# Performance work log

Hardware: AMD Instinct MI355X
Metric: run time of the kernel (lower is better)

The kernel has to match this reference:

```python
import jax, jax.numpy as jnp
from jax import lax
import numpy as np

RADIUS = 0.3
NSAMPLES = 32
SPATIAL_STRIDE = 32
TKS = 3
TSTRIDE = 2
DIM = 512
DEPTH = 4
HEADS = 8
DIM_HEAD = 64
MLP_DIM = 1024
NUM_CLASSES = 30
B, T, N = 4, 24, 4096


def setup_inputs():
    key = jax.random.key(0)
    ks = jax.random.split(key, 16)
    def w(k, shape, fan_in):
        return jax.random.normal(k, shape, jnp.float32) / np.float32(np.sqrt(fan_in))
    return {
        "xyzs": jax.random.uniform(ks[0], (B, T, N, 3), jnp.float32),
        "old_features": jax.random.normal(ks[1], (B, T, 2, N), jnp.float32),
        "conv_d_w": w(ks[2], (DIM, 4), 4),
        "conv_f_w": w(ks[3], (DIM, 2), 2),
        "pos_w": w(ks[4], (DIM, 4), 4),
        "pos_b": jnp.zeros((DIM,), jnp.float32),
        "contr_w": w(ks[5], (DIM, 4), 4),
        "contr_b": jnp.zeros((DIM,), jnp.float32),
        "ln1_s": jnp.ones((DEPTH, DIM), jnp.float32),
        "ln1_b": jnp.zeros((DEPTH, DIM), jnp.float32),
        "qkv_w": w(ks[6], (DEPTH, 3 * HEADS * DIM_HEAD, DIM), DIM),
        "out_w": w(ks[7], (DEPTH, DIM, HEADS * DIM_HEAD), HEADS * DIM_HEAD),
        "out_b": jnp.zeros((DEPTH, DIM), jnp.float32),
        "ln2_s": jnp.ones((DEPTH, DIM), jnp.float32),
        "ln2_b": jnp.zeros((DEPTH, DIM), jnp.float32),
        "ff1_w": w(ks[8], (DEPTH, MLP_DIM, DIM), DIM),
        "ff1_b": jnp.zeros((DEPTH, MLP_DIM), jnp.float32),
        "ff2_w": w(ks[9], (DEPTH, DIM, MLP_DIM), MLP_DIM),
        "ff2_b": jnp.zeros((DEPTH, DIM), jnp.float32),
        "head_ln_s": jnp.ones((DIM,), jnp.float32),
        "head_ln_b": jnp.zeros((DIM,), jnp.float32),
        "head1_w": w(ks[10], (MLP_DIM, DIM), DIM),
        "head1_b": jnp.zeros((MLP_DIM,), jnp.float32),
        "head2_w": w(ks[11], (NUM_CLASSES, MLP_DIM), MLP_DIM),
        "head2_b": jnp.zeros((NUM_CLASSES,), jnp.float32),
    }


def _fps(xyz, npoint):
    # furthest point sampling, pointnet2 semantics (start at index 0)
    n = xyz.shape[0]
    def body(carry, _):
        dist, last = carry
        d = jnp.sum((xyz - xyz[last]) ** 2, axis=-1)
        dist = jnp.minimum(dist, d)
        nxt = jnp.argmax(dist).astype(jnp.int32)
        return (dist, nxt), nxt
    init = (jnp.full((n,), 1e10, xyz.dtype), jnp.int32(0))
    _, idxs = lax.scan(body, init, None, length=npoint - 1)
    return jnp.concatenate([jnp.zeros((1,), jnp.int32), idxs])


def _ball_query(anchor, neighbor):
    # anchor [M,3], neighbor [N,3] -> [M,NSAMPLES] int32; first-k-in-radius, pad with first hit
    n = neighbor.shape[0]
    d2 = jnp.sum((anchor[:, None, :] - neighbor[None, :, :]) ** 2, axis=-1)
    pos = jnp.where(d2 < RADIUS * RADIUS, jnp.arange(n, dtype=jnp.int32), n)
    idx = -lax.top_k(-pos, NSAMPLES)[0]          # k smallest scan positions
    idx = jnp.where(idx == n, idx[:, :1], idx)   # pad with first found index
    return jnp.where(idx == n, 0, idx)           # nothing in radius -> 0


def _group(pts, idx):
    # pts [B,To,N,C], idx [B,To,M,K] -> [B,To,M,K,C]
    b, to, m, k = idx.shape
    g = jnp.take_along_axis(pts, idx.reshape(b, to, m * k)[..., None], axis=2)
    return g.reshape(b, to, m, k, pts.shape[-1])


def _p4dconv(xyzs, feats, conv_d_w, conv_f_w):
    b, t, n, _ = xyzs.shape
    m = n // SPATIAL_STRIDE
    rad = TKS // 2
    # temporal replicate padding [1,0]
    xyzs_p = jnp.concatenate([xyzs[:, :1], xyzs], axis=1)                             # [B,T+1,N,3]
    feats_p = jnp.concatenate([feats[:, :1], feats], axis=1).transpose(0, 1, 3, 2)    # [B,T+1,N,2]
    t_idx = np.arange(rad, t + 1 - rad, TSTRIDE)                                      # anchor frames (static)
    anchors = xyzs_p[:, t_idx]                                                        # [B,To,N,3]
    fps_idx = jax.vmap(jax.vmap(lambda x: _fps(x, m)))(anchors)                       # [B,To,M]
    anchor_xyz = jnp.take_along_axis(anchors, fps_idx[..., None], axis=2)             # [B,To,M,3]
    pooled = None
    for o in range(-rad, rad + 1):  # temporal kernel (small, structural)
        nb_xyz = xyzs_p[:, t_idx + o]
        nb_feat = feats_p[:, t_idx + o]
        idx = jax.vmap(jax.vmap(_ball_query))(anchor_xyz, nb_xyz)                     # [B,To,M,K]
        disp = _group(nb_xyz, idx) - anchor_xyz[:, :, :, None, :]                     # [B,To,M,K,3]
        disp4 = jnp.concatenate([disp, jnp.full(disp.shape[:-1] + (1,), float(o), disp.dtype)], axis=-1)
        d_emb = jnp.einsum('btmkc,dc->btmkd', disp4, conv_d_w)
        f_emb = jnp.einsum('btmkc,dc->btmkd', _group(nb_feat, idx), conv_f_w)
        feat = jnp.max(f_emb * d_emb, axis=3)                                          # spatial max-pool [B,To,M,D]
        pooled = feat if pooled is None else jnp.maximum(pooled, feat)                 # temporal max-pool
    return anchor_xyz, pooled


def _ln(x, s, b):
    mu = jnp.mean(x, axis=-1, keepdims=True)
    var = jnp.mean((x - mu) ** 2, axis=-1, keepdims=True)
    return (x - mu) / jnp.sqrt(var + 1e-5) * s + b


def reference(xyzs, old_features, conv_d_w, conv_f_w, pos_w, pos_b, contr_w, contr_b,
              ln1_s, ln1_b, qkv_w, out_w, out_b, ln2_s, ln2_b, ff1_w, ff1_b, ff2_w, ff2_b,
              head_ln_s, head_ln_b, head1_w, head1_b, head2_w, head2_b):
    new_xyz, feat = _p4dconv(xyzs, old_features, conv_d_w, conv_f_w)   # [B,To,M,3], [B,To,M,D]
    b, to, m, _ = new_xyz.shape
    tvals = jnp.arange(1, to + 1, dtype=new_xyz.dtype)
    xyzt = jnp.concatenate([new_xyz, jnp.broadcast_to(tvals[None, :, None, None], (b, to, m, 1))], axis=-1)
    xyzts = xyzt.reshape(b, to * m, 4)
    features = feat.reshape(b, to * m, DIM)
    pos = xyzts @ pos_w.T + pos_b                    # Conv1d(4,dim,k=1) == pointwise linear
    contrastive = xyzts @ contr_w.T + contr_b        # Linear(4,dim) on raw [x,y,z,t] tokens
    x = jax.nn.relu(pos + features)
    scale = DIM_HEAD ** -0.5
    for l in range(DEPTH):
        h = _ln(x, ln1_s[l], ln1_b[l])
        qkv = h @ qkv_w[l].T
        q, k, v = jnp.split(qkv, 3, axis=-1)
        q = q.reshape(b, -1, HEADS, DIM_HEAD)
        k = k.reshape(b, -1, HEADS, DIM_HEAD)
        v = v.reshape(b, -1, HEADS, DIM_HEAD)
        att = jax.nn.softmax(jnp.einsum('bihd,bjhd->bhij', q, k) * scale, axis=-1)
        o = jnp.einsum('bhij,bjhd->bihd', att, v).reshape(b, -1, HEADS * DIM_HEAD)
        x = x + o @ out_w[l].T + out_b[l]
        h = _ln(x, ln2_s[l], ln2_b[l])
        x = x + jax.nn.gelu(h @ ff1_w[l].T + ff1_b[l], approximate=False) @ ff2_w[l].T + ff2_b[l]
    pooled = jnp.max(x, axis=1)
    h = _ln(pooled, head_ln_s, head_ln_b)
    logits = jax.nn.gelu(h @ head1_w.T + head1_b, approximate=False) @ head2_w.T + head2_b
    return logits, contrastive, features
```

## Files before the change

### kernel.cpp

```cpp
#include <hip/hip_runtime.h>
#include <math.h>

#define BN_  4
#define TT   24
#define NN   4096
#define TO   12
#define MM   128
#define LL   (TO*MM)
#define BL   (BN_*LL)
#define DM   512
#define NH   8
#define DH   64
#define MLPD 1024
#define NC   30

#define OUT_LOGITS 0
#define OUT_CONTR  (BN_*NC)
#define OUT_FEATS  (OUT_CONTR + BL*DM)

typedef __attribute__((ext_vector_type(8))) short s16x8;
typedef __attribute__((ext_vector_type(4))) float f32x4;
#define MFMA(a,b,c) __builtin_amdgcn_mfma_f32_16x16x32_bf16(a,b,c,0,0,0)

__device__ __forceinline__ void split_bf16(float a, short &h, short &l) {
  unsigned u = __float_as_uint(a);
  h = (short)(u >> 16);
  float ah = __uint_as_float(u & 0xffff0000u);
  float al = a - ah;
  l = (short)(__float_as_uint(al) >> 16);
}

__device__ __forceinline__ void split8(float4 a, float4 b, s16x8 &h8, s16x8 &l8) {
  short h, l;
  split_bf16(a.x,h,l); h8[0]=h; l8[0]=l;
  split_bf16(a.y,h,l); h8[1]=h; l8[1]=l;
  split_bf16(a.z,h,l); h8[2]=h; l8[2]=l;
  split_bf16(a.w,h,l); h8[3]=h; l8[3]=l;
  split_bf16(b.x,h,l); h8[4]=h; l8[4]=l;
  split_bf16(b.y,h,l); h8[5]=h; l8[5]=l;
  split_bf16(b.z,h,l); h8[6]=h; l8[6]=l;
  split_bf16(b.w,h,l); h8[7]=h; l8[7]=l;
}

__device__ __forceinline__ float d2_3(float ax, float ay, float az,
                                      float bx, float by, float bz) {
#pragma clang fp contract(off)
  float dx = ax - bx, dy = ay - by, dz = az - bz;
  float dx2 = dx * dx, dy2 = dy * dy, dz2 = dz * dz;
  return (dx2 + dy2) + dz2;
}

__device__ __forceinline__ float gelu_f(float v) {
  return 0.5f * v * (1.0f + erff(v * 0.70710678118654752440f));
}

__global__ __launch_bounds__(256) void fps_kernel(const float* __restrict__ xyzs,
                                                  float* __restrict__ anchor) {
  __shared__ float sx[NN], sy[NN], sz[NN];
  __shared__ float swv[4];
  __shared__ int   swi[4];
  __shared__ int   s_next;
  int blk = blockIdx.x;
  int b = blk / TO, ti = blk - b * TO;
  int frame = 2 * ti;
  const float* src = xyzs + ((size_t)(b * TT + frame)) * NN * 3;
  int tid = threadIdx.x;
  float dist[16], px[16], py[16], pz[16];
#pragma unroll
  for (int s = 0; s < 16; ++s) {
    int p = tid + s * 256;
    px[s] = src[p * 3 + 0]; py[s] = src[p * 3 + 1]; pz[s] = src[p * 3 + 2];
    sx[p] = px[s]; sy[p] = py[s]; sz[p] = pz[s];
    dist[s] = 1e10f;
  }
  __syncthreads();
  float lx = sx[0], ly = sy[0], lz = sz[0];
  float* aout = anchor + (size_t)blk * MM * 3;
  if (tid == 0) { aout[0] = lx; aout[1] = ly; aout[2] = lz; }
  for (int j = 1; j < MM; ++j) {
    float bestv = -1.0f; int besti = 0;
#pragma unroll
    for (int s = 0; s < 16; ++s) {
      float d2 = d2_3(px[s], py[s], pz[s], lx, ly, lz);
      float dn = fminf(dist[s], d2);
      dist[s] = dn;
      if (dn > bestv) { bestv = dn; besti = tid + s * 256; }
    }
    for (int m = 1; m < 64; m <<= 1) {
      float ov = __shfl_xor(bestv, m, 64);
      int   oi = __shfl_xor(besti, m, 64);
      if (ov > bestv || (ov == bestv && oi < besti)) { bestv = ov; besti = oi; }
    }
    if ((tid & 63) == 0) { swv[tid >> 6] = bestv; swi[tid >> 6] = besti; }
    __syncthreads();
    if (tid == 0) {
      float bv = swv[0]; int bi = swi[0];
      for (int q = 1; q < 4; ++q)
        if (swv[q] > bv || (swv[q] == bv && swi[q] < bi)) { bv = swv[q]; bi = swi[q]; }
      s_next = bi;
      aout[j * 3 + 0] = sx[bi]; aout[j * 3 + 1] = sy[bi]; aout[j * 3 + 2] = sz[bi];
    }
    __syncthreads();
    int nxt = s_next;
    lx = sx[nxt]; ly = sy[nxt]; lz = sz[nxt];
  }
}

__global__ __launch_bounds__(64) void ballconv_kernel(
    const float* __restrict__ xyzs, const float* __restrict__ oldf,
    const float* __restrict__ anchor,
    const float* __restrict__ wdw, const float* __restrict__ wfw,
    float* __restrict__ dout) {
  __shared__ int   sidx[32];
  __shared__ float sdisp[32][4];
  __shared__ float sfeat[32][2];
  int blk = blockIdx.x;
  int b = blk / (TO * MM);
  int rem = blk - b * (TO * MM);
  int ti = rem / MM;
  int lane = threadIdx.x;
  const float* ap = anchor + (size_t)blk * 3;
  float ax = ap[0], ay = ap[1], az = ap[2];
  int d0 = lane * 8;
  float4 wd[8]; float2 wf[8];
#pragma unroll
  for (int jd = 0; jd < 8; ++jd) {
    wd[jd] = *(const float4*)(wdw + (d0 + jd) * 4);
    wf[jd] = *(const float2*)(wfw + (d0 + jd) * 2);
  }
  float fmx[8];
#pragma unroll
  for (int jd = 0; jd < 8; ++jd) fmx[jd] = -INFINITY;

  for (int o = -1; o <= 1; ++o) {
    int tp = 1 + 2 * ti + o;
    int orig = (tp == 0) ? 0 : tp - 1;
    const float* nx = xyzs + ((size_t)(b * TT + orig)) * NN * 3;
    const float* nf = oldf + ((size_t)(b * TT + orig)) * 2 * NN;
    int cnt = 0;
    for (int base = 0; base < NN && cnt < 32; base += 64) {
      int p = base + lane;
      float d2 = d2_3(ax, ay, az, nx[p * 3], nx[p * 3 + 1], nx[p * 3 + 2]);
      bool in = d2 < 0.09f;
      unsigned long long mask = __ballot(in);
      int pos = __popcll(mask & ((1ull << lane) - 1ull));
      if (in && (cnt + pos) < 32) sidx[cnt + pos] = p;
      cnt += __popcll(mask);
    }
    __syncthreads();
    int used = cnt < 32 ? cnt : 32;
    if (lane < 32 && lane >= used) sidx[lane] = (used > 0) ? sidx[0] : 0;
    __syncthreads();
    if (lane < 32) {
      int p = sidx[lane];
      sdisp[lane][0] = nx[p * 3 + 0] - ax;
      sdisp[lane][1] = nx[p * 3 + 1] - ay;
      sdisp[lane][2] = nx[p * 3 + 2] - az;
      sdisp[lane][3] = (float)o;
      sfeat[lane][0] = nf[p];
      sfeat[lane][1] = nf[NN + p];
    }
    __syncthreads();
    for (int k = 0; k < 32; ++k) {
      float p0 = sdisp[k][0], p1 = sdisp[k][1], p2 = sdisp[k][2], p3 = sdisp[k][3];
      float f0 = sfeat[k][0], f1 = sfeat[k][1];
#pragma unroll
      for (int jd = 0; jd < 8; ++jd) {
        float de = wd[jd].x * p0 + wd[jd].y * p1 + wd[jd].z * p2 + wd[jd].w * p3;
        float fe = wf[jd].x * f0 + wf[jd].y * f1;
        fmx[jd] = fmaxf(fmx[jd], fe * de);
      }
    }
    __syncthreads();
  }
  float* fout = dout + OUT_FEATS + (size_t)blk * DM + d0;
#pragma unroll
  for (int jd = 0; jd < 8; jd += 4)
    *(float4*)(fout + jd) = make_float4(fmx[jd], fmx[jd + 1], fmx[jd + 2], fmx[jd + 3]);
}

__global__ __launch_bounds__(256) void posx_kernel(
    const float* __restrict__ anchor,
    const float* __restrict__ pw, const float* __restrict__ pb,
    const float* __restrict__ cw, const float* __restrict__ cb,
    float* __restrict__ dout, float* __restrict__ x) {
  int idx = blockIdx.x * 256 + threadIdx.x;
  int bl = idx >> 9, d = idx & 511;
  int ti = (bl % LL) / MM;
  const float* ap = anchor + (size_t)bl * 3;
  float c0 = ap[0], c1 = ap[1], c2 = ap[2], c3 = (float)(ti + 1);
  float4 pwv = *(const float4*)(pw + d * 4);
  float4 cwv = *(const float4*)(cw + d * 4);
  float pos = pwv.x * c0 + pwv.y * c1 + pwv.z * c2 + pwv.w * c3 + pb[d];
  float con = cwv.x * c0 + cwv.y * c1 + cwv.z * c2 + cwv.w * c3 + cb[d];
  dout[OUT_CONTR + (size_t)idx] = con;
  float v = pos + dout[OUT_FEATS + (size_t)idx];
  x[idx] = v > 0.0f ? v : 0.0f;
}

__global__ __launch_bounds__(64) void ln_split_kernel(
    const float* __restrict__ x, const float* __restrict__ gs,
    const float* __restrict__ gb, short* __restrict__ oh, short* __restrict__ ol) {
  int row = blockIdx.x, lane = threadIdx.x;
  const float* xr = x + (size_t)row * DM + lane * 8;
  float4 v0 = *(const float4*)xr;
  float4 v1 = *(const float4*)(xr + 4);
  float v[8] = {v0.x, v0.y, v0.z, v0.w, v1.x, v1.y, v1.z, v1.w};
  float s = 0.f;
#pragma unroll
  for (int j = 0; j < 8; ++j) s += v[j];
  for (int m = 1; m < 64; m <<= 1) s += __shfl_xor(s, m, 64);
  float mu = s * (1.0f / DM);
  float d[8], ss = 0.f;
#pragma unroll
  for (int j = 0; j < 8; ++j) { d[j] = v[j] - mu; ss += d[j] * d[j]; }
  for (int m = 1; m < 64; m <<= 1) ss += __shfl_xor(ss, m, 64);
  float rs = 1.0f / sqrtf(ss * (1.0f / DM) + 1e-5f);
  const float* gsr = gs + lane * 8;
  const float* gbr = gb + lane * 8;
  s16x8 hv, lv;
#pragma unroll
  for (int j = 0; j < 8; ++j) {
    float f = d[j] * rs * gsr[j] + gbr[j];
    short h, l; split_bf16(f, h, l);
    hv[j] = h; lv[j] = l;
  }
  *(s16x8*)(oh + (size_t)row * DM + lane * 8) = hv;
  *(s16x8*)(ol + (size_t)row * DM + lane * 8) = lv;
}

__global__ __launch_bounds__(64) void ln_kernel(
    const float* __restrict__ x, const float* __restrict__ gs,
    const float* __restrict__ gb, float* __restrict__ out) {
  int row = blockIdx.x, lane = threadIdx.x;
  const float* xr = x + (size_t)row * DM + lane * 8;
  float4 v0 = *(const float4*)xr;
  float4 v1 = *(const float4*)(xr + 4);
  float v[8] = {v0.x, v0.y, v0.z, v0.w, v1.x, v1.y, v1.z, v1.w};
  float s = 0.f;
#pragma unroll
  for (int j = 0; j < 8; ++j) s += v[j];
  for (int m = 1; m < 64; m <<= 1) s += __shfl_xor(s, m, 64);
  float mu = s * (1.0f / DM);
  float d[8], ss = 0.f;
#pragma unroll
  for (int j = 0; j < 8; ++j) { d[j] = v[j] - mu; ss += d[j] * d[j]; }
  for (int m = 1; m < 64; m <<= 1) ss += __shfl_xor(ss, m, 64);
  float rs = 1.0f / sqrtf(ss * (1.0f / DM) + 1e-5f);
  const float* gsr = gs + lane * 8;
  const float* gbr = gb + lane * 8;
  float* orow = out + (size_t)row * DM + lane * 8;
  float r[8];
#pragma unroll
  for (int j = 0; j < 8; ++j) r[j] = d[j] * rs * gsr[j] + gbr[j];
  *(float4*)orow       = make_float4(r[0], r[1], r[2], r[3]);
  *(float4*)(orow + 4) = make_float4(r[4], r[5], r[6], r[7]);
}

template <int EPI>
__global__ __launch_bounds__(256) void mgemm_kernel(
    const short* __restrict__ Ah, const short* __restrict__ Al,
    const float* __restrict__ W,
    const float* __restrict__ bias, const float* __restrict__ res,
    float* __restrict__ Cf, short* __restrict__ Ch, short* __restrict__ Cl,
    int M, int N, int K) {
  __shared__ short As[2][128 * 40];
  __shared__ short Ws[2][128 * 40];
  int tid = threadIdx.x;
  int lane = tid & 63, w = tid >> 6;
  int wr = w >> 1, wc = w & 1;
  int row0 = blockIdx.y * 128, col0 = blockIdx.x * 128;
  int srow = tid >> 1, skc = (tid & 1) * 16;
  const short* Ahp = Ah + (size_t)(row0 + srow) * K + skc;
  const short* Alp = Al + (size_t)(row0 + srow) * K + skc;
  const float* Wp  = W  + (size_t)(col0 + srow) * K + skc;
  int fr = lane & 15, fk = (lane >> 4) * 8;
  f32x4 acc[16];
#pragma unroll
  for (int i = 0; i < 16; ++i) acc[i] = (f32x4){0.f, 0.f, 0.f, 0.f};
  s16x8 rA0 = *(const s16x8*)(Ahp);
  s16x8 rA1 = *(const s16x8*)(Ahp + 8);
  s16x8 rA2 = *(const s16x8*)(Alp);
  s16x8 rA3 = *(const s16x8*)(Alp + 8);
  float4 rW0 = *(const float4*)(Wp);
  float4 rW1 = *(const float4*)(Wp + 4);
  float4 rW2 = *(const float4*)(Wp + 8);
  float4 rW3 = *(const float4*)(Wp + 12);
  for (int ks = 0; ks < K; ks += 32) {
    __syncthreads();
    *(s16x8*)&As[0][srow * 40 + skc]     = rA0;
    *(s16x8*)&As[0][srow * 40 + skc + 8] = rA1;
    *(s16x8*)&As[1][srow * 40 + skc]     = rA2;
    *(s16x8*)&As[1][srow * 40 + skc + 8] = rA3;
    s16x8 wh0, wl0, wh1, wl1;
    split8(rW0, rW1, wh0, wl0);
    split8(rW2, rW3, wh1, wl1);
    *(s16x8*)&Ws[0][srow * 40 + skc]     = wh0;
    *(s16x8*)&Ws[0][srow * 40 + skc + 8] = wh1;
    *(s16x8*)&Ws[1][srow * 40 + skc]     = wl0;
    *(s16x8*)&Ws[1][srow * 40 + skc + 8] = wl1;
    __syncthreads();
    if (ks + 32 < K) {
      rA0 = *(const s16x8*)(Ahp + ks + 32);
      rA1 = *(const s16x8*)(Ahp + ks + 40);
      rA2 = *(const s16x8*)(Alp + ks + 32);
      rA3 = *(const s16x8*)(Alp + ks + 40);
      rW0 = *(const float4*)(Wp + ks + 32);
      rW1 = *(const float4*)(Wp + ks + 36);
      rW2 = *(const float4*)(Wp + ks + 40);
      rW3 = *(const float4*)(Wp + ks + 44);
    }
    s16x8 bh_[4], bl_[4];
#pragma unroll
    for (int t = 0; t < 4; ++t) {
      bh_[t] = *(const s16x8*)&Ws[0][(wc * 64 + t * 16 + fr) * 40 + fk];
      bl_[t] = *(const s16x8*)&Ws[1][(wc * 64 + t * 16 + fr) * 40 + fk];
    }
#pragma unroll
    for (int a = 0; a < 4; ++a) {
      s16x8 ah_ = *(const s16x8*)&As[0][(wr * 64 + a * 16 + fr) * 40 + fk];
      s16x8 al_ = *(const s16x8*)&As[1][(wr * 64 + a * 16 + fr) * 40 + fk];
#pragma unroll
      for (int t = 0; t < 4; ++t) {
        f32x4 c = acc[a * 4 + t];
        c = MFMA(ah_, bh_[t], c);
        c = MFMA(ah_, bl_[t], c);
        c = MFMA(al_, bh_[t], c);
        acc[a * 4 + t] = c;
      }
    }
  }
  int fq = lane >> 4;
#pragma unroll
  for (int a = 0; a < 4; ++a) {
#pragma unroll
    for (int t = 0; t < 4; ++t) {
#pragma unroll
      for (int r = 0; r < 4; ++r) {
        int row = row0 + wr * 64 + a * 16 + fq * 4 + r;
        int c   = col0 + wc * 64 + t * 16 + fr;
        size_t off = (size_t)row * N + c;
        float v = acc[a * 4 + t][r];
        if (EPI >= 2) v += bias[c];
        if (EPI == 2) {
          v = gelu_f(v);
          short h, l; split_bf16(v, h, l);
          Ch[off] = h; Cl[off] = l;
        } else if (EPI == 3) {
          v += res[off];
          Cf[off] = v;
        } else {
          short h, l; split_bf16(v, h, l);
          Ch[off] = h; Cl[off] = l;
        }
      }
    }
  }
}

__global__ __launch_bounds__(256) void mattn_kernel(
    const short* __restrict__ qh, const short* __restrict__ ql,
    short* __restrict__ oh, short* __restrict__ ol) {
  __shared__ short KV[2][64 * 72];
  __shared__ short Ps[2][64 * 72];
  int it = blockIdx.x, bh = blockIdx.y;
  int b = bh >> 3, h = bh & 7;
  int tid = threadIdx.x, lane = tid & 63, w = tid >> 6;
  int fr = lane & 15, fq = lane >> 4, fk = fq * 8;
  size_t rowbase = (size_t)b * LL;
  const int QS = 3 * DM;
  s16x8 qfh[2], qfl[2];
  {
    size_t qoff = (size_t)(rowbase + it * 64 + w * 16 + fr) * QS + h * DH;
    qfh[0] = *(const s16x8*)(qh + qoff + fk);
    qfh[1] = *(const s16x8*)(qh + qoff + 32 + fk);
    qfl[0] = *(const s16x8*)(ql + qoff + fk);
    qfl[1] = *(const s16x8*)(ql + qoff + 32 + fk);
  }
  float m_i[4], l_i[4];
  f32x4 oac[4];
#pragma unroll
  for (int r = 0; r < 4; ++r) { m_i[r] = -INFINITY; l_i[r] = 0.f; }
#pragma unroll
  for (int t = 0; t < 4; ++t) oac[t] = (f32x4){0.f, 0.f, 0.f, 0.f};
  int kjr = tid >> 2, kc0 = (tid & 3) * 16;
  int vd = tid & 63, vj0 = (tid >> 6) * 16;
  for (int jt = 0; jt < LL / 64; ++jt) {
    size_t kbase = (size_t)(rowbase + jt * 64 + kjr) * QS + DM + h * DH + kc0;
    s16x8 k0 = *(const s16x8*)(qh + kbase);
    s16x8 k1 = *(const s16x8*)(qh + kbase + 8);
    s16x8 k2 = *(const s16x8*)(ql + kbase);
    s16x8 k3 = *(const s16x8*)(ql + kbase + 8);
    __syncthreads();
    *(s16x8*)&KV[0][kjr * 72 + kc0]     = k0;
    *(s16x8*)&KV[0][kjr * 72 + kc0 + 8] = k1;
    *(s16x8*)&KV[1][kjr * 72 + kc0]     = k2;
    *(s16x8*)&KV[1][kjr * 72 + kc0 + 8] = k3;
    __syncthreads();
    f32x4 s[4];
#pragma unroll
    for (int t = 0; t < 4; ++t) s[t] = (f32x4){0.f, 0.f, 0.f, 0.f};
#pragma unroll
    for (int ks = 0; ks < 2; ++ks) {
#pragma unroll
      for (int t = 0; t < 4; ++t) {
        s16x8 kh_ = *(const s16x8*)&KV[0][(t * 16 + fr) * 72 + ks * 32 + fk];
        s16x8 kl_ = *(const s16x8*)&KV[1][(t * 16 + fr) * 72 + ks * 32 + fk];
        s[t] = MFMA(qfh[ks], kh_, s[t]);
        s[t] = MFMA(qfh[ks], kl_, s[t]);
        s[t] = MFMA(qfl[ks], kh_, s[t]);
      }
    }
    size_t vbase = (size_t)(rowbase + jt * 64 + vj0) * QS + 2 * DM + h * DH + vd;
    s16x8 vh0, vh1, vl0, vl1;
#pragma unroll
    for (int q = 0; q < 8; ++q) {
      vh0[q] = qh[vbase + (size_t)q * QS];
      vh1[q] = qh[vbase + (size_t)(q + 8) * QS];
      vl0[q] = ql[vbase + (size_t)q * QS];
      vl1[q] = ql[vbase + (size_t)(q + 8) * QS];
    }
#pragma unroll
    for (int r = 0; r < 4; ++r) {
      float s0 = s[0][r] * 0.125f, s1 = s[1][r] * 0.125f;
      float s2 = s[2][r] * 0.125f, s3 = s[3][r] * 0.125f;
      float mr = fmaxf(fmaxf(s0, s1), fmaxf(s2, s3));
      mr = fmaxf(mr, __shfl_xor(mr, 1, 64));
      mr = fmaxf(mr, __shfl_xor(mr, 2, 64));
      mr = fmaxf(mr, __shfl_xor(mr, 4, 64));
      mr = fmaxf(mr, __shfl_xor(mr, 8, 64));
      float mn = fmaxf(m_i[r], mr);
      float al = expf(m_i[r] - mn);
      float p0 = expf(s0 - mn), p1 = expf(s1 - mn);
      float p2 = expf(s2 - mn), p3 = expf(s3 - mn);
      float ps = p0 + p1 + p2 + p3;
      ps += __shfl_xor(ps, 1, 64); ps += __shfl_xor(ps, 2, 64);
      ps += __shfl_xor(ps, 4, 64); ps += __shfl_xor(ps, 8, 64);
      l_i[r] = l_i[r] * al + ps;
      m_i[r] = mn;
      oac[0][r] *= al; oac[1][r] *= al; oac[2][r] *= al; oac[3][r] *= al;
      int prow = (w * 16 + fq * 4 + r) * 72;
      short hh, ll;
      split_bf16(p0, hh, ll); Ps[0][prow + fr]      = hh; Ps[1][prow + fr]      = ll;
      split_bf16(p1, hh, ll); Ps[0][prow + 16 + fr] = hh; Ps[1][prow + 16 + fr] = ll;
      split_bf16(p2, hh, ll); Ps[0][prow + 32 + fr] = hh; Ps[1][prow + 32 + fr] = ll;
      split_bf16(p3, hh, ll); Ps[0][prow + 48 + fr] = hh; Ps[1][prow + 48 + fr] = ll;
    }
    __syncthreads();
    *(s16x8*)&KV[0][vd * 72 + vj0]     = vh0;
    *(s16x8*)&KV[0][vd * 72 + vj0 + 8] = vh1;
    *(s16x8*)&KV[1][vd * 72 + vj0]     = vl0;
    *(s16x8*)&KV[1][vd * 72 + vj0 + 8] = vl1;
    __syncthreads();
#pragma unroll
    for (int ks = 0; ks < 2; ++ks) {
      s16x8 ph_ = *(const s16x8*)&Ps[0][(w * 16 + fr) * 72 + ks * 32 + fk];
      s16x8 pl_ = *(const s16x8*)&Ps[1][(w * 16 + fr) * 72 + ks * 32 + fk];
#pragma unroll
      for (int t = 0; t < 4; ++t) {
        s16x8 vh_ = *(const s16x8*)&KV[0][(t * 16 + fr) * 72 + ks * 32 + fk];
        s16x8 vl_ = *(const s16x8*)&KV[1][(t * 16 + fr) * 72 + ks * 32 + fk];
        oac[t] = MFMA(ph_, vh_, oac[t]);
        oac[t] = MFMA(ph_, vl_, oac[t]);
        oac[t] = MFMA(pl_, vh_, oac[t]);
      }
    }
  }
#pragma unroll
  for (int r = 0; r < 4; ++r) {
    float inv = 1.0f / l_i[r];
    size_t row = rowbase + it * 64 + w * 16 + fq * 4 + r;
#pragma unroll
    for (int t = 0; t < 4; ++t) {
      float v = oac[t][r] * inv;
      short hh, ll; split_bf16(v, hh, ll);
      size_t off = row * DM + h * DH + t * 16 + fr;
      oh[off] = hh; ol[off] = ll;
    }
  }
}

__global__ __launch_bounds__(256) void poolmax1_kernel(const float* __restrict__ x,
                                                       float* __restrict__ partial) {
  int ch = blockIdx.x, b = blockIdx.y, tid = threadIdx.x;
  const float* p = x + ((size_t)b * LL + ch * 128) * DM;
  float m0 = -INFINITY, m1 = -INFINITY;
#pragma unroll 4
  for (int l = 0; l < 128; ++l) {
    m0 = fmaxf(m0, p[(size_t)l * DM + tid]);
    m1 = fmaxf(m1, p[(size_t)l * DM + tid + 256]);
  }
  partial[(size_t)(b * TO + ch) * DM + tid] = m0;
  partial[(size_t)(b * TO + ch) * DM + tid + 256] = m1;
}

__global__ __launch_bounds__(256) void poolmax2_kernel(const float* __restrict__ partial,
                                                       float* __restrict__ pooled) {
  int idx = blockIdx.x * 256 + threadIdx.x;
  int b = idx >> 9, d = idx & 511;
  float m = -INFINITY;
#pragma unroll
  for (int c = 0; c < TO; ++c) m = fmaxf(m, partial[(size_t)(b * TO + c) * DM + d]);
  pooled[idx] = m;
}

__global__ __launch_bounds__(256) void head1_kernel(const float* __restrict__ lnp,
                                                    const float* __restrict__ w,
                                                    const float* __restrict__ bb,
                                                    float* __restrict__ hid) {
  int idx = blockIdx.x * 256 + threadIdx.x;
  int b = idx >> 10, n = idx & 1023;
  const float* xr = lnp + (size_t)b * DM;
  const float* wr = w + (size_t)n * DM;
  float s = 0.f;
  for (int k = 0; k < DM; k += 4) {
    float4 xv = *(const float4*)(xr + k);
    float4 wv = *(const float4*)(wr + k);
    s += xv.x * wv.x + xv.y * wv.y + xv.z * wv.z + xv.w * wv.w;
  }
  hid[idx] = gelu_f(s + bb[n]);
}

__global__ __launch_bounds__(128) void head2_kernel(const float* __restrict__ hid,
                                                    const float* __restrict__ w,
                                                    const float* __restrict__ bb,
                                                    float* __restrict__ dout) {
  int t = threadIdx.x;
  if (t < BN_ * NC) {
    int b = t / NC, n = t - b * NC;
    const float* xr = hid + (size_t)b * MLPD;
    const float* wr = w + (size_t)n * MLPD;
    float s = 0.f;
    for (int k = 0; k < MLPD; k += 4) {
      float4 xv = *(const float4*)(xr + k);
      float4 wv = *(const float4*)(wr + k);
      s += xv.x * wv.x + xv.y * wv.y + xv.z * wv.z + xv.w * wv.w;
    }
    dout[OUT_LOGITS + t] = s + bb[n];
  }
}

extern "C" void kernel_launch(void* const* d_in, const int* in_sizes, int n_in,
                              void* d_out, int out_size, void* d_ws, size_t ws_size,
                              hipStream_t stream) {
  (void)in_sizes; (void)n_in; (void)out_size; (void)ws_size;
  const float* xyzs     = (const float*)d_in[0];
  const float* oldf     = (const float*)d_in[1];
  const float* conv_d_w = (const float*)d_in[2];
  const float* conv_f_w = (const float*)d_in[3];
  const float* pos_w    = (const float*)d_in[4];
  const float* pos_b    = (const float*)d_in[5];
  const float* contr_w  = (const float*)d_in[6];
  const float* contr_b  = (const float*)d_in[7];
  const float* ln1_s    = (const float*)d_in[8];
  const float* ln1_b    = (const float*)d_in[9];
  const float* qkv_w    = (const float*)d_in[10];
  const float* out_w    = (const float*)d_in[11];
  const float* out_b    = (const float*)d_in[12];
  const float* ln2_s    = (const float*)d_in[13];
  const float* ln2_b    = (const float*)d_in[14];
  const float* ff1_w    = (const float*)d_in[15];
  const float* ff1_b    = (const float*)d_in[16];
  const float* ff2_w    = (const float*)d_in[17];
  const float* ff2_b    = (const float*)d_in[18];
  const float* hl_s     = (const float*)d_in[19];
  const float* hl_b     = (const float*)d_in[20];
  const float* h1_w     = (const float*)d_in[21];
  const float* h1_b     = (const float*)d_in[22];
  const float* h2_w     = (const float*)d_in[23];
  const float* h2_b     = (const float*)d_in[24];
  float* dout = (float*)d_out;
  char* base = (char*)d_ws;

  float* anchor = (float*)base;            base += (size_t)BN_ * TO * MM * 3 * 4;
  float* x      = (float*)base;            base += (size_t)BL * DM * 4;
  short* qkvh   = (short*)base;            base += (size_t)BL * 3 * DM * 2;
  short* qkvl   = (short*)base;            base += (size_t)BL * 3 * DM * 2;
  short* atnh   = (short*)base;            base += (size_t)BL * DM * 2;
  short* atnl   = (short*)base;            base += (size_t)BL * DM * 2;
  short* hh     = (short*)base;            base += (size_t)BL * DM * 2;
  short* hl     = (short*)base;            base += (size_t)BL * DM * 2;
  float* partial= (float*)base;            base += (size_t)BN_ * TO * DM * 4;
  float* pooled = (float*)base;            base += (size_t)BN_ * DM * 4;
  float* lnp    = (float*)base;            base += (size_t)BN_ * DM * 4;
  float* hid    = (float*)base;            base += (size_t)BN_ * MLPD * 4;
  short* fh = qkvh;
  short* fl = qkvl;

  fps_kernel<<<BN_ * TO, 256, 0, stream>>>(xyzs, anchor);
  ballconv_kernel<<<BN_ * TO * MM, 64, 0, stream>>>(xyzs, oldf, anchor, conv_d_w, conv_f_w, dout);
  posx_kernel<<<(BL * DM) / 256, 256, 0, stream>>>(anchor, pos_w, pos_b, contr_w, contr_b, dout, x);

  for (int l = 0; l < 4; ++l) {
    ln_split_kernel<<<BL, 64, 0, stream>>>(x, ln1_s + l * DM, ln1_b + l * DM, hh, hl);
    mgemm_kernel<1><<<dim3(3 * DM / 128, BL / 128), 256, 0, stream>>>(
        hh, hl, qkv_w + (size_t)l * 3 * DM * DM, nullptr, nullptr,
        nullptr, qkvh, qkvl, BL, 3 * DM, DM);
    mattn_kernel<<<dim3(LL / 64, BN_ * NH), 256, 0, stream>>>(qkvh, qkvl, atnh, atnl);
    mgemm_kernel<3><<<dim3(DM / 128, BL / 128), 256, 0, stream>>>(
        atnh, atnl, out_w + (size_t)l * DM * DM, out_b + l * DM, x,
        x, nullptr, nullptr, BL, DM, DM);
    ln_split_kernel<<<BL, 64, 0, stream>>>(x, ln2_s + l * DM, ln2_b + l * DM, hh, hl);
    mgemm_kernel<2><<<dim3(MLPD / 128, BL / 128), 256, 0, stream>>>(
        hh, hl, ff1_w + (size_t)l * MLPD * DM, ff1_b + l * MLPD, nullptr,
        nullptr, fh, fl, BL, MLPD, DM);
    mgemm_kernel<3><<<dim3(DM / 128, BL / 128), 256, 0, stream>>>(
        fh, fl, ff2_w + (size_t)l * DM * MLPD, ff2_b + l * DM, x,
        x, nullptr, nullptr, BL, DM, MLPD);
  }

  poolmax1_kernel<<<dim3(TO, BN_), 256, 0, stream>>>(x, partial);
  poolmax2_kernel<<<(BN_ * DM) / 256, 256, 0, stream>>>(partial, pooled);
  ln_kernel<<<BN_, 64, 0, stream>>>(pooled, hl_s, hl_b, lnp);
  head1_kernel<<<(BN_ * MLPD) / 256, 256, 0, stream>>>(lnp, h1_w, h1_b, hid);
  head2_kernel<<<1, 128, 0, stream>>>(hid, h2_w, h2_b, dout);
}
```

Before: 1.651 ms.

## Pre-split weights to bf16, write V transposed, and streamline FPS argmax

Adds a kernel that splits all transformer weights into bf16 hi/lo arrays once per call, so the GEMMs load shorts directly and skip the per-tile split. The QKV GEMM epilogue now writes V into a per-head transposed layout. This lets the attention kernel load V fragments straight from global memory, dropping the strided scalar gathers and one shared-memory round trip with its barriers. FPS packs distance and index into a 64-bit key, which removes the single-thread final reduction and one barrier per iteration, at the cost of extra workspace and an extra weight-split pass.

Measured after the change: 1.756 ms. +6.4%, slower.

```diff
diff --git a/kernel.cpp b/kernel.cpp
--- a/kernel.cpp
+++ b/kernel.cpp
@@ -18,6 +18,16 @@
 #define OUT_CONTR  (BN_*NC)
 #define OUT_FEATS  (OUT_CONTR + BL*DM)
 
+#define NWQ   3145728
+#define NWO   1048576
+#define NWF1  2097152
+#define NWF2  2097152
+#define WQOFF   0
+#define WOOFF   (NWQ)
+#define WF1OFF  (NWQ+NWO)
+#define WF2OFF  (NWQ+NWO+NWF1)
+#define WTOT    (NWQ+NWO+NWF1+NWF2)
+
 typedef __attribute__((ext_vector_type(8))) short s16x8;
 typedef __attribute__((ext_vector_type(4))) float f32x4;
 #define MFMA(a,b,c) __builtin_amdgcn_mfma_f32_16x16x32_bf16(a,b,c,0,0,0)
@@ -30,18 +40,6 @@
   l = (short)(__float_as_uint(al) >> 16);
 }
 
-__device__ __forceinline__ void split8(float4 a, float4 b, s16x8 &h8, s16x8 &l8) {
-  short h, l;
-  split_bf16(a.x,h,l); h8[0]=h; l8[0]=l;
-  split_bf16(a.y,h,l); h8[1]=h; l8[1]=l;
-  split_bf16(a.z,h,l); h8[2]=h; l8[2]=l;
-  split_bf16(a.w,h,l); h8[3]=h; l8[3]=l;
-  split_bf16(b.x,h,l); h8[4]=h; l8[4]=l;
-  split_bf16(b.y,h,l); h8[5]=h; l8[5]=l;
-  split_bf16(b.z,h,l); h8[6]=h; l8[6]=l;
-  split_bf16(b.w,h,l); h8[7]=h; l8[7]=l;
-}
-
 __device__ __forceinline__ float d2_3(float ax, float ay, float az,
                                       float bx, float by, float bz) {
 #pragma clang fp contract(off)
@@ -54,16 +52,28 @@
   return 0.5f * v * (1.0f + erff(v * 0.70710678118654752440f));
 }
 
+__global__ __launch_bounds__(256) void splitw_kernel(
+    const float* __restrict__ qkv_w, const float* __restrict__ out_w,
+    const float* __restrict__ ff1_w, const float* __restrict__ ff2_w,
+    short* __restrict__ wh, short* __restrict__ wl) {
+  int i = blockIdx.x * 256 + threadIdx.x;
+  const float* src; int off;
+  if (i < WOOFF)        { src = qkv_w; off = i; }
+  else if (i < WF1OFF)  { src = out_w; off = i - WOOFF; }
+  else if (i < WF2OFF)  { src = ff1_w; off = i - WF1OFF; }
+  else                  { src = ff2_w; off = i - WF2OFF; }
+  float v = src[off];
+  short h, l; split_bf16(v, h, l);
+  wh[i] = h; wl[i] = l;
+}
+
 __global__ __launch_bounds__(256) void fps_kernel(const float* __restrict__ xyzs,
                                                   float* __restrict__ anchor) {
   __shared__ float sx[NN], sy[NN], sz[NN];
-  __shared__ float swv[4];
-  __shared__ int   swi[4];
-  __shared__ int   s_next;
+  __shared__ unsigned long long skey[2][4];
   int blk = blockIdx.x;
   int b = blk / TO, ti = blk - b * TO;
-  int frame = 2 * ti;
-  const float* src = xyzs + ((size_t)(b * TT + frame)) * NN * 3;
+  const float* src = xyzs + ((size_t)(b * TT + 2 * ti)) * NN * 3;
   int tid = threadIdx.x;
   float dist[16], px[16], py[16], pz[16];
 #pragma unroll
@@ -78,31 +88,31 @@
   float* aout = anchor + (size_t)blk * MM * 3;
   if (tid == 0) { aout[0] = lx; aout[1] = ly; aout[2] = lz; }
   for (int j = 1; j < MM; ++j) {
-    float bestv = -1.0f; int besti = 0;
+    unsigned long long best = 0;
 #pragma unroll
     for (int s = 0; s < 16; ++s) {
       float d2 = d2_3(px[s], py[s], pz[s], lx, ly, lz);
       float dn = fminf(dist[s], d2);
       dist[s] = dn;
-      if (dn > bestv) { bestv = dn; besti = tid + s * 256; }
-    }
+      unsigned long long key = ((unsigned long long)__float_as_uint(dn) << 12)
+                               | (unsigned)(4095 - (tid + s * 256));
+      best = key > best ? key : best;
+    }
+#pragma unroll
     for (int m = 1; m < 64; m <<= 1) {
-      float ov = __shfl_xor(bestv, m, 64);
-      int   oi = __shfl_xor(besti, m, 64);
-      if (ov > bestv || (ov == bestv && oi < besti)) { bestv = ov; besti = oi; }
-    }
-    if ((tid & 63) == 0) { swv[tid >> 6] = bestv; swi[tid >> 6] = besti; }
-    __syncthreads();
-    if (tid == 0) {
-      float bv = swv[0]; int bi = swi[0];
-      for (int q = 1; q < 4; ++q)
-        if (swv[q] > bv || (swv[q] == bv && swi[q] < bi)) { bv = swv[q]; bi = swi[q]; }
-      s_next = bi;
-      aout[j * 3 + 0] = sx[bi]; aout[j * 3 + 1] = sy[bi]; aout[j * 3 + 2] = sz[bi];
-    }
-    __syncthreads();
-    int nxt = s_next;
-    lx = sx[nxt]; ly = sy[nxt]; lz = sz[nxt];
+      unsigned long long o = __shfl_xor(best, m, 64);
+      best = o > best ? o : best;
+    }
+    if ((tid & 63) == 0) skey[j & 1][tid >> 6] = best;
+    __syncthreads();
+    unsigned long long b0 = skey[j & 1][0], b1 = skey[j & 1][1];
+    unsigned long long b2 = skey[j & 1][2], b3 = skey[j & 1][3];
+    unsigned long long bb = b0 > b1 ? b0 : b1;
+    unsigned long long cc = b2 > b3 ? b2 : b3;
+    bb = bb > cc ? bb : cc;
+    int bi = 4095 - (int)(bb & 0xFFFull);
+    lx = sx[bi]; ly = sy[bi]; lz = sz[bi];
+    if (tid == 0) { aout[j * 3 + 0] = lx; aout[j * 3 + 1] = ly; aout[j * 3 + 2] = lz; }
   }
 }
 
@@ -260,9 +270,10 @@
 template <int EPI>
 __global__ __launch_bounds__(256) void mgemm_kernel(
     const short* __restrict__ Ah, const short* __restrict__ Al,
-    const float* __restrict__ W,
+    const short* __restrict__ Wh, const short* __restrict__ Wl,
     const float* __restrict__ bias, const float* __restrict__ res,
     float* __restrict__ Cf, short* __restrict__ Ch, short* __restrict__ Cl,
+    short* __restrict__ vTh, short* __restrict__ vTl,
     int M, int N, int K) {
   __shared__ short As[2][128 * 40];
   __shared__ short Ws[2][128 * 40];
@@ -273,7 +284,8 @@
   int srow = tid >> 1, skc = (tid & 1) * 16;
   const short* Ahp = Ah + (size_t)(row0 + srow) * K + skc;
   const short* Alp = Al + (size_t)(row0 + srow) * K + skc;
-  const float* Wp  = W  + (size_t)(col0 + srow) * K + skc;
+  const short* Whp = Wh + (size_t)(col0 + srow) * K + skc;
+  const short* Wlp = Wl + (size_t)(col0 + srow) * K + skc;
   int fr = lane & 15, fk = (lane >> 4) * 8;
   f32x4 acc[16];
 #pragma unroll
@@ -282,33 +294,30 @@
   s16x8 rA1 = *(const s16x8*)(Ahp + 8);
   s16x8 rA2 = *(const s16x8*)(Alp);
   s16x8 rA3 = *(const s16x8*)(Alp + 8);
-  float4 rW0 = *(const float4*)(Wp);
-  float4 rW1 = *(const float4*)(Wp + 4);
-  float4 rW2 = *(const float4*)(Wp + 8);
-  float4 rW3 = *(const float4*)(Wp + 12);
+  s16x8 rW0 = *(const s16x8*)(Whp);
+  s16x8 rW1 = *(const s16x8*)(Whp + 8);
+  s16x8 rW2 = *(const s16x8*)(Wlp);
+  s16x8 rW3 = *(const s16x8*)(Wlp + 8);
   for (int ks = 0; ks < K; ks += 32) {
     __syncthreads();
     *(s16x8*)&As[0][srow * 40 + skc]     = rA0;
     *(s16x8*)&As[0][srow * 40 + skc + 8] = rA1;
     *(s16x8*)&As[1][srow * 40 + skc]     = rA2;
     *(s16x8*)&As[1][srow * 40 + skc + 8] = rA3;
-    s16x8 wh0, wl0, wh1, wl1;
-    split8(rW0, rW1, wh0, wl0);
-    split8(rW2, rW3, wh1, wl1);
-    *(s16x8*)&Ws[0][srow * 40 + skc]     = wh0;
-    *(s16x8*)&Ws[0][srow * 40 + skc + 8] = wh1;
-    *(s16x8*)&Ws[1][srow * 40 + skc]     = wl0;
-    *(s16x8*)&Ws[1][srow * 40 + skc + 8] = wl1;
+    *(s16x8*)&Ws[0][srow * 40 + skc]     = rW0;
+    *(s16x8*)&Ws[0][srow * 40 + skc + 8] = rW1;
+    *(s16x8*)&Ws[1][srow * 40 + skc]     = rW2;
+    *(s16x8*)&Ws[1][srow * 40 + skc + 8] = rW3;
     __syncthreads();
     if (ks + 32 < K) {
       rA0 = *(const s16x8*)(Ahp + ks + 32);
       rA1 = *(const s16x8*)(Ahp + ks + 40);
       rA2 = *(const s16x8*)(Alp + ks + 32);
       rA3 = *(const s16x8*)(Alp + ks + 40);
-      rW0 = *(const float4*)(Wp + ks + 32);
-      rW1 = *(const float4*)(Wp + ks + 36);
-      rW2 = *(const float4*)(Wp + ks + 40);
-      rW3 = *(const float4*)(Wp + ks + 44);
+      rW0 = *(const s16x8*)(Whp + ks + 32);
+      rW1 = *(const s16x8*)(Whp + ks + 40);
+      rW2 = *(const s16x8*)(Wlp + ks + 32);
+      rW3 = *(const s16x8*)(Wlp + ks + 40);
     }
     s16x8 bh_[4], bl_[4];
 #pragma unroll
@@ -331,52 +340,83 @@
     }
   }
   int fq = lane >> 4;
-#pragma unroll
-  for (int a = 0; a < 4; ++a) {
-#pragma unroll
-    for (int t = 0; t < 4; ++t) {
-#pragma unroll
-      for (int r = 0; r < 4; ++r) {
-        int row = row0 + wr * 64 + a * 16 + fq * 4 + r;
-        int c   = col0 + wc * 64 + t * 16 + fr;
-        size_t off = (size_t)row * N + c;
-        float v = acc[a * 4 + t][r];
-        if (EPI >= 2) v += bias[c];
-        if (EPI == 2) {
-          v = gelu_f(v);
-          short h, l; split_bf16(v, h, l);
-          Ch[off] = h; Cl[off] = l;
-        } else if (EPI == 3) {
-          v += res[off];
-          Cf[off] = v;
+  if (EPI == 1) {
+    int bidx = row0 / LL;
+    int j0 = row0 - bidx * LL + wr * 64;
+#pragma unroll
+    for (int a = 0; a < 4; ++a) {
+#pragma unroll
+      for (int t = 0; t < 4; ++t) {
+        int c = col0 + wc * 64 + t * 16 + fr;
+        f32x4 v = acc[a * 4 + t];
+        if (col0 < 1024) {
+#pragma unroll
+          for (int r = 0; r < 4; ++r) {
+            int row = row0 + wr * 64 + a * 16 + fq * 4 + r;
+            size_t off = (size_t)row * 1024 + c;
+            short h, l; split_bf16(v[r], h, l);
+            Ch[off] = h; Cl[off] = l;
+          }
         } else {
-          short h, l; split_bf16(v, h, l);
-          Ch[off] = h; Cl[off] = l;
+          int vcol = c - 1024;
+          size_t vidx = ((size_t)(bidx * 8 + (vcol >> 6)) * 64 + (vcol & 63)) * LL
+                        + j0 + a * 16 + fq * 4;
+          short4 hv, lv;
+          short h, l;
+          split_bf16(v[0], h, l); hv.x = h; lv.x = l;
+          split_bf16(v[1], h, l); hv.y = h; lv.y = l;
+          split_bf16(v[2], h, l); hv.z = h; lv.z = l;
+          split_bf16(v[3], h, l); hv.w = h; lv.w = l;
+          *(short4*)(vTh + vidx) = hv;
+          *(short4*)(vTl + vidx) = lv;
         }
       }
     }
+  } else {
+#pragma unroll
+    for (int a = 0; a < 4; ++a) {
+#pragma unroll
+      for (int t = 0; t < 4; ++t) {
+#pragma unroll
+        for (int r = 0; r < 4; ++r) {
+          int row = row0 + wr * 64 + a * 16 + fq * 4 + r;
+          int c   = col0 + wc * 64 + t * 16 + fr;
+          size_t off = (size_t)row * N + c;
+          float v = acc[a * 4 + t][r] + bias[c];
+          if (EPI == 2) {
+            v = gelu_f(v);
+            short h, l; split_bf16(v, h, l);
+            Ch[off] = h; Cl[off] = l;
+          } else {
+            Cf[off] = v + res[off];
+          }
+        }
+      }
+    }
   }
 }
 
 __global__ __launch_bounds__(256) void mattn_kernel(
-    const short* __restrict__ qh, const short* __restrict__ ql,
+    const short* __restrict__ qkh, const short* __restrict__ qkl,
+    const short* __restrict__ vTh, const short* __restrict__ vTl,
     short* __restrict__ oh, short* __restrict__ ol) {
-  __shared__ short KV[2][64 * 72];
+  __shared__ short Ks[2][64 * 72];
   __shared__ short Ps[2][64 * 72];
   int it = blockIdx.x, bh = blockIdx.y;
   int b = bh >> 3, h = bh & 7;
   int tid = threadIdx.x, lane = tid & 63, w = tid >> 6;
   int fr = lane & 15, fq = lane >> 4, fk = fq * 8;
   size_t rowbase = (size_t)b * LL;
-  const int QS = 3 * DM;
   s16x8 qfh[2], qfl[2];
   {
-    size_t qoff = (size_t)(rowbase + it * 64 + w * 16 + fr) * QS + h * DH;
-    qfh[0] = *(const s16x8*)(qh + qoff + fk);
-    qfh[1] = *(const s16x8*)(qh + qoff + 32 + fk);
-    qfl[0] = *(const s16x8*)(ql + qoff + fk);
-    qfl[1] = *(const s16x8*)(ql + qoff + 32 + fk);
-  }
+    size_t qoff = (size_t)(rowbase + it * 64 + w * 16 + fr) * 1024 + h * DH;
+    qfh[0] = *(const s16x8*)(qkh + qoff + fk);
+    qfh[1] = *(const s16x8*)(qkh + qoff + 32 + fk);
+    qfl[0] = *(const s16x8*)(qkl + qoff + fk);
+    qfl[1] = *(const s16x8*)(qkl + qoff + 32 + fk);
+  }
+  const short* vbh = vTh + (size_t)(b * 8 + h) * 64 * LL;
+  const short* vbl = vTl + (size_t)(b * 8 + h) * 64 * LL;
   float m_i[4], l_i[4];
   f32x4 oac[4];
 #pragma unroll
@@ -384,18 +424,17 @@
 #pragma unroll
   for (int t = 0; t < 4; ++t) oac[t] = (f32x4){0.f, 0.f, 0.f, 0.f};
   int kjr = tid >> 2, kc0 = (tid & 3) * 16;
-  int vd = tid & 63, vj0 = (tid >> 6) * 16;
   for (int jt = 0; jt < LL / 64; ++jt) {
-    size_t kbase = (size_t)(rowbase + jt * 64 + kjr) * QS + DM + h * DH + kc0;
-    s16x8 k0 = *(const s16x8*)(qh + kbase);
-    s16x8 k1 = *(const s16x8*)(qh + kbase + 8);
-    s16x8 k2 = *(const s16x8*)(ql + kbase);
-    s16x8 k3 = *(const s16x8*)(ql + kbase + 8);
-    __syncthreads();
-    *(s16x8*)&KV[0][kjr * 72 + kc0]     = k0;
-    *(s16x8*)&KV[0][kjr * 72 + kc0 + 8] = k1;
-    *(s16x8*)&KV[1][kjr * 72 + kc0]     = k2;
-    *(s16x8*)&KV[1][kjr * 72 + kc0 + 8] = k3;
+    size_t kbase = (size_t)(rowbase + jt * 64 + kjr) * 1024 + 512 + h * DH + kc0;
+    s16x8 k0 = *(const s16x8*)(qkh + kbase);
+    s16x8 k1 = *(const s16x8*)(qkh + kbase + 8);
+    s16x8 k2 = *(const s16x8*)(qkl + kbase);
+    s16x8 k3 = *(const s16x8*)(qkl + kbase + 8);
+    __syncthreads();
+    *(s16x8*)&Ks[0][kjr * 72 + kc0]     = k0;
+    *(s16x8*)&Ks[0][kjr * 72 + kc0 + 8] = k1;
+    *(s16x8*)&Ks[1][kjr * 72 + kc0]     = k2;
+    *(s16x8*)&Ks[1][kjr * 72 + kc0 + 8] = k3;
     __syncthreads();
     f32x4 s[4];
 #pragma unroll
@@ -404,21 +443,22 @@
     for (int ks = 0; ks < 2; ++ks) {
 #pragma unroll
       for (int t = 0; t < 4; ++t) {
-        s16x8 kh_ = *(const s16x8*)&KV[0][(t * 16 + fr) * 72 + ks * 32 + fk];
-        s16x8 kl_ = *(const s16x8*)&KV[1][(t * 16 + fr) * 72 + ks * 32 + fk];
+        s16x8 kh_ = *(const s16x8*)&Ks[0][(t * 16 + fr) * 72 + ks * 32 + fk];
+        s16x8 kl_ = *(const s16x8*)&Ks[1][(t * 16 + fr) * 72 + ks * 32 + fk];
         s[t] = MFMA(qfh[ks], kh_, s[t]);
         s[t] = MFMA(qfh[ks], kl_, s[t]);
         s[t] = MFMA(qfl[ks], kh_, s[t]);
       }
     }
-    size_t vbase = (size_t)(rowbase + jt * 64 + vj0) * QS + 2 * DM + h * DH + vd;
-    s16x8 vh0, vh1, vl0, vl1;
-#pragma unroll
-    for (int q = 0; q < 8; ++q) {
-      vh0[q] = qh[vbase + (size_t)q * QS];
-      vh1[q] = qh[vbase + (size_t)(q + 8) * QS];
-      vl0[q] = ql[vbase + (size_t)q * QS];
-      vl1[q] = ql[vbase + (size_t)(q + 8) * QS];
+    s16x8 vh_[2][4], vl_[2][4];
+#pragma unroll
+    for (int ks = 0; ks < 2; ++ks) {
+#pragma unroll
+      for (int t = 0; t < 4; ++t) {
+        size_t voff = (size_t)(t * 16 + fr) * LL + jt * 64 + ks * 32 + fk;
+        vh_[ks][t] = *(const s16x8*)(vbh + voff);
+        vl_[ks][t] = *(const s16x8*)(vbl + voff);
+      }
     }
 #pragma unroll
     for (int r = 0; r < 4; ++r) {
@@ -440,29 +480,21 @@
       m_i[r] = mn;
       oac[0][r] *= al; oac[1][r] *= al; oac[2][r] *= al; oac[3][r] *= al;
       int prow = (w * 16 + fq * 4 + r) * 72;
-      short hh, ll;
-      split_bf16(p0, hh, ll); Ps[0][prow + fr]      = hh; Ps[1][prow + fr]      = ll;
-      split_bf16(p1, hh, ll); Ps[0][prow + 16 + fr] = hh; Ps[1][prow + 16 + fr] = ll;
-      split_bf16(p2, hh, ll); Ps[0][prow + 32 + fr] = hh; Ps[1][prow + 32 + fr] = ll;
-      split_bf16(p3, hh, ll); Ps[0][prow + 48 + fr] = hh; Ps[1][prow + 48 + fr] = ll;
-    }
-    __syncthreads();
-    *(s16x8*)&KV[0][vd * 72 + vj0]     = vh0;
-    *(s16x8*)&KV[0][vd * 72 + vj0 + 8] = vh1;
-    *(s16x8*)&KV[1][vd * 72 + vj0]     = vl0;
-    *(s16x8*)&KV[1][vd * 72 + vj0 + 8] = vl1;
-    __syncthreads();
+      short hh_, ll_;
+      split_bf16(p0, hh_, ll_); Ps[0][prow + fr]      = hh_; Ps[1][prow + fr]      = ll_;
+      split_bf16(p1, hh_, ll_); Ps[0][prow + 16 + fr] = hh_; Ps[1][prow + 16 + fr] = ll_;
+      split_bf16(p2, hh_, ll_); Ps[0][prow + 32 + fr] = hh_; Ps[1][prow + 32 + fr] = ll_;
+      split_bf16(p3, hh_, ll_); Ps[0][prow + 48 + fr] = hh_; Ps[1][prow + 48 + fr] = ll_;
+    }
 #pragma unroll
     for (int ks = 0; ks < 2; ++ks) {
       s16x8 ph_ = *(const s16x8*)&Ps[0][(w * 16 + fr) * 72 + ks * 32 + fk];
       s16x8 pl_ = *(const s16x8*)&Ps[1][(w * 16 + fr) * 72 + ks * 32 + fk];
 #pragma unroll
       for (int t = 0; t < 4; ++t) {
-        s16x8 vh_ = *(const s16x8*)&KV[0][(t * 16 + fr) * 72 + ks * 32 + fk];
-        s16x8 vl_ = *(const s16x8*)&KV[1][(t * 16 + fr) * 72 + ks * 32 + fk];
-        oac[t] = MFMA(ph_, vh_, oac[t]);
-        oac[t] = MFMA(ph_, vl_, oac[t]);
-        oac[t] = MFMA(pl_, vh_, oac[t]);
+        oac[t] = MFMA(ph_, vh_[ks][t], oac[t]);
+        oac[t] = MFMA(ph_, vl_[ks][t], oac[t]);
+        oac[t] = MFMA(pl_, vh_[ks][t], oac[t]);
       }
     }
   }
@@ -473,9 +505,9 @@
 #pragma unroll
     for (int t = 0; t < 4; ++t) {
       float v = oac[t][r] * inv;
-      short hh, ll; split_bf16(v, hh, ll);
+      short hh_, ll_; split_bf16(v, hh_, ll_);
       size_t off = row * DM + h * DH + t * 16 + fr;
-      oh[off] = hh; ol[off] = ll;
+      oh[off] = hh_; ol[off] = ll_;
     }
   }
 }
@@ -571,42 +603,48 @@
   const float* h2_b     = (const float*)d_in[24];
   float* dout = (float*)d_out;
   char* base = (char*)d_ws;
-
-  float* anchor = (float*)base;            base += (size_t)BN_ * TO * MM * 3 * 4;
-  float* x      = (float*)base;            base += (size_t)BL * DM * 4;
-  short* qkvh   = (short*)base;            base += (size_t)BL * 3 * DM * 2;
-  short* qkvl   = (short*)base;            base += (size_t)BL * 3 * DM * 2;
-  short* atnh   = (short*)base;            base += (size_t)BL * DM * 2;
-  short* atnl   = (short*)base;            base += (size_t)BL * DM * 2;
-  short* hh     = (short*)base;            base += (size_t)BL * DM * 2;
-  short* hl     = (short*)base;            base += (size_t)BL * DM * 2;
-  float* partial= (float*)base;            base += (size_t)BN_ * TO * DM * 4;
-  float* pooled = (float*)base;            base += (size_t)BN_ * DM * 4;
-  float* lnp    = (float*)base;            base += (size_t)BN_ * DM * 4;
-  float* hid    = (float*)base;            base += (size_t)BN_ * MLPD * 4;
+  auto alloc = [&](size_t bytes) { char* p = base; base += (bytes + 255) & ~(size_t)255; return p; };
+
+  float* anchor = (float*)alloc((size_t)BN_ * TO * MM * 3 * 4);
+  float* x      = (float*)alloc((size_t)BL * DM * 4);
+  short* qkvh   = (short*)alloc((size_t)BL * 1024 * 2);
+  short* qkvl   = (short*)alloc((size_t)BL * 1024 * 2);
+  short* vTh    = (short*)alloc((size_t)BN_ * NH * DH * LL * 2);
+  short* vTl    = (short*)alloc((size_t)BN_ * NH * DH * LL * 2);
+  short* atnh   = (short*)alloc((size_t)BL * DM * 2);
+  short* atnl   = (short*)alloc((size_t)BL * DM * 2);
+  short* hh     = (short*)alloc((size_t)BL * DM * 2);
+  short* hl     = (short*)alloc((size_t)BL * DM * 2);
+  short* wsh    = (short*)alloc((size_t)WTOT * 2);
+  short* wsl    = (short*)alloc((size_t)WTOT * 2);
+  float* partial= (float*)alloc((size_t)BN_ * TO * DM * 4);
+  float* pooled = (float*)alloc((size_t)BN_ * DM * 4);
+  float* lnp    = (float*)alloc((size_t)BN_ * DM * 4);
+  float* hid    = (float*)alloc((size_t)BN_ * MLPD * 4);
   short* fh = qkvh;
   short* fl = qkvl;
 
+  splitw_kernel<<<WTOT / 256, 256, 0, stream>>>(qkv_w, out_w, ff1_w, ff2_w, wsh, wsl);
   fps_kernel<<<BN_ * TO, 256, 0, stream>>>(xyzs, anchor);
   ballconv_kernel<<<BN_ * TO * MM, 64, 0, stream>>>(xyzs, oldf, anchor, conv_d_w, conv_f_w, dout);
   posx_kernel<<<(BL * DM) / 256, 256, 0, stream>>>(anchor, pos_w, pos_b, contr_w, contr_b, dout, x);
 
   for (int l = 0; l < 4; ++l) {
     ln_split_kernel<<<BL, 64, 0, stream>>>(x, ln1_s + l * DM, ln1_b + l * DM, hh, hl);
-    mgemm_kernel<1><<<dim3(3 * DM / 128, BL / 128), 256, 0, stream>>>(
-        hh, hl, qkv_w + (size_t)l * 3 * DM * DM, nullptr, nullptr,
-        nullptr, qkvh, qkvl, BL, 3 * DM, DM);
-    mattn_kernel<<<dim3(LL / 64, BN_ * NH), 256, 0, stream>>>(qkvh, qkvl, atnh, atnl);
+    mgemm_kernel<1><<<dim3(1536 / 128, BL / 128), 256, 0, stream>>>(
+        hh, hl, wsh + WQOFF + (size_t)l * 786432, wsl + WQOFF + (size_t)l * 786432,
+        nullptr, nullptr, nullptr, qkvh, qkvl, vTh, vTl, BL, 1536, DM);
+    mattn_kernel<<<dim3(LL / 64, BN_ * NH), 256, 0, stream>>>(qkvh, qkvl, vTh, vTl, atnh, atnl);
     mgemm_kernel<3><<<dim3(DM / 128, BL / 128), 256, 0, stream>>>(
-        atnh, atnl, out_w + (size_t)l * DM * DM, out_b + l * DM, x,
-        x, nullptr, nullptr, BL, DM, DM);
+        atnh, atnl, wsh + WOOFF + (size_t)l * 262144, wsl + WOOFF + (size_t)l * 262144,
+        out_b + l * DM, x, x, nullptr, nullptr, nullptr, nullptr, BL, DM, DM);
     ln_split_kernel<<<BL, 64, 0, stream>>>(x, ln2_s + l * DM, ln2_b + l * DM, hh, hl);
     mgemm_kernel<2><<<dim3(MLPD / 128, BL / 128), 256, 0, stream>>>(
-        hh, hl, ff1_w + (size_t)l * MLPD * DM, ff1_b + l * MLPD, nullptr,
-        nullptr, fh, fl, BL, MLPD, DM);
+        hh, hl, wsh + WF1OFF + (size_t)l * 524288, wsl + WF1OFF + (size_t)l * 524288,
+        ff1_b + l * MLPD, nullptr, nullptr, fh, fl, nullptr, nullptr, BL, MLPD, DM);
     mgemm_kernel<3><<<dim3(DM / 128, BL / 128), 256, 0, stream>>>(
-        fh, fl, ff2_w + (size_t)l * DM * MLPD, ff2_b + l * DM, x,
-        x, nullptr, nullptr, BL, DM, MLPD);
+        fh, fl, wsh + WF2OFF + (size_t)l * 524288, wsl + WF2OFF + (size_t)l * 524288,
+        ff2_b + l * DM, x, x, nullptr, nullptr, nullptr, nullptr, BL, DM, MLPD);
   }
 
   poolmax1_kernel<<<dim3(TO, BN_), 256, 0, stream>>>(x, partial);
```
